# Performance work log

Measured on AMD Instinct MI355X. Metric: run time of the kernel, lower is better.

The kernel has to match this reference:

```python
import jax, jax.numpy as jnp
import numpy as np

D = 256          # out_feats
H = 4            # n_heads
DH = D // H      # per-head feats
S = 8192         # number of snapshots (segments)
PER = 32         # edges (selected papers) per snapshot
E = S * PER      # total edges
NP = 200000      # number of papers
ST = 10          # snapshot_types (embedding has ST+1 rows, padding_idx=-1)
SLOPE = 0.01     # LeakyReLU negative slope (torch default)


def setup_inputs() -> dict:
    key = jax.random.key(0)
    ks = jax.random.split(key, 20)
    sc = 1.0 / np.sqrt(D)
    papers = jax.random.normal(ks[0], (NP, D), dtype=jnp.float32)
    snapshots = jax.random.normal(ks[1], (S, D), dtype=jnp.float32)
    cur_snapshot_types = jax.random.randint(ks[2], (S,), 0, ST + 1, dtype=jnp.int32)
    is_cite = jax.random.randint(ks[3], (NP,), 0, 2, dtype=jnp.int32)
    selected_indicator = jax.random.randint(ks[4], (E,), 0, NP, dtype=jnp.int64)
    # contiguous sorted segment ids, PER edges per snapshot (matches valid_num_nodes)
    index = jnp.repeat(jnp.arange(S, dtype=jnp.int32), PER)
    # linear layers (torch Linear: y = x @ W.T + b)
    W_src = jax.random.normal(ks[5], (D, D), dtype=jnp.float32) * sc
    b_src = jnp.zeros((D,), dtype=jnp.float32)
    W_dst = jax.random.normal(ks[6], (D, D), dtype=jnp.float32) * sc
    b_dst = jnp.zeros((D,), dtype=jnp.float32)
    W_out = jax.random.normal(ks[7], (D, D), dtype=jnp.float32) * sc
    b_out = jnp.zeros((D,), dtype=jnp.float32)
    # node attr embeddings (2 rows, padding_idx=0 -> row 0 zero)
    emb_cite = jax.random.normal(ks[8], (2, D), dtype=jnp.float32).at[0].set(0.0)
    emb_ref = jax.random.normal(ks[9], (2, D), dtype=jnp.float32).at[0].set(0.0)
    emb_target = jax.random.normal(ks[10], (2, D), dtype=jnp.float32).at[0].set(0.0)
    # snapshot type embedding (ST+1 rows, padding_idx=-1 -> last row zero)
    snapshot_emb = jax.random.normal(ks[11], (ST + 1, D), dtype=jnp.float32).at[-1].set(0.0)
    # attention vectors, xavier_normal with relu gain
    gain = np.sqrt(2.0)
    std = gain * np.sqrt(2.0 / (H * DH + 1))
    attn = jax.random.normal(ks[12], (1, H, DH), dtype=jnp.float32) * std
    attn_t = jax.random.normal(ks[13], (1, H, DH), dtype=jnp.float32) * std
    return {
        "papers": papers, "snapshots": snapshots,
        "W_src": W_src, "b_src": b_src, "W_dst": W_dst, "b_dst": b_dst,
        "W_out": W_out, "b_out": b_out,
        "emb_cite": emb_cite, "emb_ref": emb_ref, "emb_target": emb_target,
        "snapshot_emb": snapshot_emb, "attn": attn, "attn_t": attn_t,
        "cur_snapshot_types": cur_snapshot_types, "is_cite": is_cite,
        "selected_indicator": selected_indicator, "index": index,
    }


def _leaky(x):
    return jnp.where(x >= 0, x, SLOPE * x)


def reference(papers, snapshots, W_src, b_src, W_dst, b_dst, W_out, b_out,
              emb_cite, emb_ref, emb_target, snapshot_emb, attn, attn_t,
              cur_snapshot_types, is_cite, selected_indicator, index):
    # gather src papers per edge: [E, D]
    h_src = papers[selected_indicator]
    feat_src = (h_src @ W_src.T + b_src).reshape(-1, H, DH)          # [E,H,DH]
    ic = is_cite[selected_indicator]
    # original uses 'is_cite' indices for all three attr embeddings (faithful)
    src_type_h = (emb_cite[ic] + emb_ref[ic] + emb_target[ic]).reshape(-1, H, DH)
    dst_type_h = snapshot_emb[cur_snapshot_types].reshape(-1, H, DH)  # [S,H,DH]
    feat_dst = (snapshots @ W_dst.T + b_dst).reshape(-1, H, DH)[index]  # [E,H,DH]
    # per-edge attention logits
    e = (_leaky(feat_src + feat_dst) * attn).sum(axis=-1)             # [E,H]
    et = (_leaky(src_type_h + dst_type_h[index]) * attn_t).sum(axis=-1)
    e = e + et
    # segment (edge) softmax over destination snapshots
    m = jax.lax.stop_gradient(jax.ops.segment_max(e, index, num_segments=S))
    ex = jnp.exp(e - m[index])
    den = jax.ops.segment_sum(ex, index, num_segments=S)
    a = (ex / den[index])[..., None]                                  # [E,H,1]
    # weighted segment-sum aggregation
    x = feat_src * a
    sum_out = jax.ops.segment_sum(x, index, num_segments=S).reshape(S, D)
    return sum_out @ W_out.T + b_out
```

## Files before the change

kernel.cpp:

```cpp
#include <hip/hip_runtime.h>
#include <hip/hip_fp16.h>
#include <type_traits>

#define NSNAP 8192
#define PER 32
#define SLOPE 0.01f

using half8   = __attribute__((ext_vector_type(8))) _Float16;
using floatx4 = __attribute__((ext_vector_type(4))) float;

__device__ __forceinline__ float leaky(float x) { return x >= 0.f ? x : SLOPE * x; }

__device__ __forceinline__ unsigned pack2(float a, float b) {
    __half2 h = __floats2half2_rn(a, b);
    return *reinterpret_cast<unsigned*>(&h);
}

template <typename AT, typename OT, bool DO_PACK>
__global__ __launch_bounds__(256) void gemm64(const AT* __restrict__ A,
                                              const float* __restrict__ W,
                                              const float* __restrict__ bias,
                                              OT* __restrict__ Cout, int M,
                                              const float* __restrict__ Wsrc,
                                              _Float16* __restrict__ Wh) {
    if constexpr (DO_PACK) {
        if (blockIdx.y == 4) {
            const int t = blockIdx.x * 256 + threadIdx.x;
            const int lane = t & 63;
            const int wj = (t >> 6) & 15;
            const int k0 = t >> 10;
            const int n = (wj >> 2) * 64 + (wj & 3) * 16 + (lane & 15);
            const int k = k0 * 32 + (lane >> 4) * 8;
            const float4 v0 = *(const float4*)(Wsrc + (long)n * 256 + k);
            const float4 v1 = *(const float4*)(Wsrc + (long)n * 256 + k + 4);
            *(uint4*)(Wh + (long)t * 8) = make_uint4(pack2(v0.x, v0.y), pack2(v0.z, v0.w),
                                                     pack2(v1.x, v1.y), pack2(v1.z, v1.w));
            return;
        }
    }
    constexpr int LDA = 40;
    __shared__ _Float16 Asl[64 * LDA];
    __shared__ _Float16 Wsl[64 * LDA];

    const int m0 = blockIdx.x * 64;
    const int n0 = blockIdx.y * 64;
    const int tid = threadIdx.x;
    const int lane = tid & 63;
    const int wave = tid >> 6;
    const int wm = (wave & 1) * 32;
    const int wn = (wave >> 1) * 32;
    const int l15 = lane & 15;
    const int quad = lane >> 4;

    floatx4 acc[2][2];
#pragma unroll
    for (int i = 0; i < 2; i++)
#pragma unroll
        for (int j = 0; j < 2; j++) acc[i][j] = (floatx4)0.f;

    for (int k0 = 0; k0 < 256; k0 += 32) {
        __syncthreads();
#pragma unroll
        for (int it = 0; it < 2; ++it) {
            const int idx = tid + it * 256;
            const int row = idx >> 3;
            const int c4 = idx & 7;
            if constexpr (std::is_same_v<AT, float>) {
                const float4 v = *(const float4*)(A + (long)(m0 + row) * 256 + k0 + c4 * 4);
                *(uint2*)(&Asl[row * LDA + c4 * 4]) = make_uint2(pack2(v.x, v.y), pack2(v.z, v.w));
            } else {
                const uint2 v = *(const uint2*)(A + (long)(m0 + row) * 256 + k0 + c4 * 4);
                *(uint2*)(&Asl[row * LDA + c4 * 4]) = v;
            }
            const float4 w = *(const float4*)(W + (long)(n0 + row) * 256 + k0 + c4 * 4);
            *(uint2*)(&Wsl[row * LDA + c4 * 4]) = make_uint2(pack2(w.x, w.y), pack2(w.z, w.w));
        }
        __syncthreads();

        half8 af[2], bf[2];
#pragma unroll
        for (int i = 0; i < 2; i++)
            af[i] = *reinterpret_cast<const half8*>(&Asl[(wm + i * 16 + l15) * LDA + quad * 8]);
#pragma unroll
        for (int j = 0; j < 2; j++)
            bf[j] = *reinterpret_cast<const half8*>(&Wsl[(wn + j * 16 + l15) * LDA + quad * 8]);
#pragma unroll
        for (int i = 0; i < 2; i++)
#pragma unroll
            for (int j = 0; j < 2; j++)
                acc[i][j] = __builtin_amdgcn_mfma_f32_16x16x32_f16(af[i], bf[j], acc[i][j], 0, 0, 0);
    }

#pragma unroll
    for (int j = 0; j < 2; j++) {
        const int gcol = n0 + wn + j * 16 + l15;
        const float bv = bias[gcol];
#pragma unroll
        for (int i = 0; i < 2; i++) {
            const int rbase = m0 + wm + i * 16 + quad * 4;
#pragma unroll
            for (int r = 0; r < 4; r++) {
                const float v = acc[i][j][r] + bv;
                if constexpr (std::is_same_v<OT, __half>)
                    Cout[(long)(rbase + r) * 256 + gcol] = __float2half(v);
                else
                    Cout[(long)(rbase + r) * 256 + gcol] = v;
            }
        }
    }
}

__global__ __launch_bounds__(256, 2) void fused_attn(
    const float* __restrict__ papers, const _Float16* __restrict__ Wh,
    const float* __restrict__ b_src, const float* __restrict__ F,
    const float* __restrict__ emb_cite, const float* __restrict__ emb_ref,
    const float* __restrict__ emb_target, const float* __restrict__ snap_emb,
    const float* __restrict__ attn, const float* __restrict__ attn_t,
    const int* __restrict__ types, const int* __restrict__ is_cite,
    const int* __restrict__ sel, __half* __restrict__ SO) {
    __shared__ _Float16 Asl[64 * 256];
    __shared__ int ic_l[64];

    const int tid = threadIdx.x;
    const int lane = tid & 63;
    const int wave = tid >> 6;
    const int l15 = lane & 15;
    const int quad = lane >> 4;
    const int sbase = blockIdx.x * 2;
    const int ebase = blockIdx.x * 64;

    if (tid < 64) ic_l[tid] = is_cite[sel[ebase + tid]];

    {
        const int row = wave * 16 + l15;
        const long arow = (long)sel[ebase + row];
        const float* src = papers + arow * 256;
#pragma unroll
        for (int m = 0; m < 16; m++) {
            const float4 v = *(const float4*)(src + m * 16 + quad * 4);
            const int c8 = m * 2 + (quad >> 1);
            const int slot = (c8 >> 2) * 256 + wave * 64 + (c8 & 3) * 16 + l15;
            *(uint2*)(&Asl[slot * 8 + (quad & 1) * 4]) =
                make_uint2(pack2(v.x, v.y), pack2(v.z, v.w));
        }
    }
    __syncthreads();

    floatx4 acc[4][4];
#pragma unroll
    for (int i = 0; i < 4; i++)
#pragma unroll
        for (int j = 0; j < 4; j++) acc[i][j] = (floatx4)0.f;

    for (int k0 = 0; k0 < 8; k0++) {
        half8 af[4], bf[4];
#pragma unroll
        for (int i = 0; i < 4; i++)
            af[i] = *reinterpret_cast<const half8*>(&Asl[(k0 * 256 + i * 64 + lane) * 8]);
#pragma unroll
        for (int j = 0; j < 4; j++)
            bf[j] = *reinterpret_cast<const half8*>(Wh + ((k0 * 16 + wave * 4 + j) * 64 + lane) * 8);
#pragma unroll
        for (int i = 0; i < 4; i++)
#pragma unroll
            for (int j = 0; j < 4; j++)
                acc[i][j] = __builtin_amdgcn_mfma_f32_16x16x32_f16(af[i], bf[j], acc[i][j], 0, 0, 0);
    }

    float bsrc_j[4], attn_j[4], F0_j[4], F1_j[4];
#pragma unroll
    for (int j = 0; j < 4; j++) {
        const int col = 64 * wave + j * 16 + l15;
        bsrc_j[j] = b_src[col];
        attn_j[j] = attn[col];
        F0_j[j] = F[(long)sbase * 256 + col];
        F1_j[j] = F[(long)(sbase + 1) * 256 + col];
    }
#pragma unroll
    for (int i = 0; i < 4; i++)
#pragma unroll
        for (int j = 0; j < 4; j++)
#pragma unroll
            for (int r = 0; r < 4; r++) acc[i][j][r] += bsrc_j[j];

    const int D = 64 * wave + lane;
    const float at_d = attn_t[D];
    const float src0 = emb_cite[D] + emb_ref[D] + emb_target[D];
    const float src1 = emb_cite[256 + D] + emb_ref[256 + D] + emb_target[256 + D];
    float et[2][2];
#pragma unroll
    for (int sn = 0; sn < 2; sn++) {
        const float dstt = snap_emb[types[sbase + sn] * 256 + D];
        float p0 = leaky(src0 + dstt) * at_d;
        float p1 = leaky(src1 + dstt) * at_d;
#pragma unroll
        for (int off = 32; off; off >>= 1) {
            p0 += __shfl_xor(p0, off);
            p1 += __shfl_xor(p1, off);
        }
        et[sn][0] = p0;
        et[sn][1] = p1;
    }

    float lg[4][4];
#pragma unroll
    for (int i = 0; i < 4; i++) {
        const int sn = i >> 1;
#pragma unroll
        for (int r = 0; r < 4; r++) {
            float p = 0.f;
#pragma unroll
            for (int j = 0; j < 4; j++)
                p += leaky(acc[i][j][r] + (sn == 0 ? F0_j[j] : F1_j[j])) * attn_j[j];
#pragma unroll
            for (int off = 1; off <= 8; off <<= 1) p += __shfl_xor(p, off);
            const int row = i * 16 + quad * 4 + r;
            lg[i][r] = p + et[sn][ic_l[row]];
        }
    }

    float aw[4][4];
#pragma unroll
    for (int sn = 0; sn < 2; sn++) {
        float m = -3.4e38f;
#pragma unroll
        for (int ii = 0; ii < 2; ii++)
#pragma unroll
            for (int r = 0; r < 4; r++) m = fmaxf(m, lg[sn * 2 + ii][r]);
        m = fmaxf(m, __shfl_xor(m, 16));
        m = fmaxf(m, __shfl_xor(m, 32));
        float den = 0.f;
#pragma unroll
        for (int ii = 0; ii < 2; ii++)
#pragma unroll
            for (int r = 0; r < 4; r++) {
                const float ex = __expf(lg[sn * 2 + ii][r] - m);
                aw[sn * 2 + ii][r] = ex;
                den += ex;
            }
        den += __shfl_xor(den, 16);
        den += __shfl_xor(den, 32);
        const float inv = 1.f / den;
#pragma unroll
        for (int ii = 0; ii < 2; ii++)
#pragma unroll
            for (int r = 0; r < 4; r++) aw[sn * 2 + ii][r] *= inv;
    }

#pragma unroll
    for (int sn = 0; sn < 2; sn++) {
#pragma unroll
        for (int j = 0; j < 4; j++) {
            float o = 0.f;
#pragma unroll
            for (int ii = 0; ii < 2; ii++)
#pragma unroll
                for (int r = 0; r < 4; r++) o += aw[sn * 2 + ii][r] * acc[sn * 2 + ii][j][r];
            o += __shfl_xor(o, 16);
            o += __shfl_xor(o, 32);
            if (quad == sn)
                SO[(long)(sbase + sn) * 256 + 64 * wave + j * 16 + l15] = __float2half(o);
        }
    }
}

extern "C" void kernel_launch(void* const* d_in, const int* in_sizes, int n_in,
                              void* d_out, int out_size, void* d_ws, size_t ws_size,
                              hipStream_t stream) {
    const float* papers     = (const float*)d_in[0];
    const float* snapshots  = (const float*)d_in[1];
    const float* W_src      = (const float*)d_in[2];
    const float* b_src      = (const float*)d_in[3];
    const float* W_dst      = (const float*)d_in[4];
    const float* b_dst      = (const float*)d_in[5];
    const float* W_out      = (const float*)d_in[6];
    const float* b_out      = (const float*)d_in[7];
    const float* emb_cite   = (const float*)d_in[8];
    const float* emb_ref    = (const float*)d_in[9];
    const float* emb_target = (const float*)d_in[10];
    const float* snap_emb   = (const float*)d_in[11];
    const float* attn       = (const float*)d_in[12];
    const float* attn_t     = (const float*)d_in[13];
    const int* types        = (const int*)d_in[14];
    const int* is_cite      = (const int*)d_in[15];
    const int* sel          = (const int*)d_in[16];

    char* ws = (char*)d_ws;
    float*     F    = (float*)ws;
    __half*    SO   = (__half*)(ws + 8388608);
    _Float16*  Wh   = (_Float16*)(ws + 12582912);

    gemm64<float, float, true><<<dim3(128, 5), 256, 0, stream>>>(snapshots, W_dst, b_dst, F,
                                                                 NSNAP, W_src, Wh);
    fused_attn<<<NSNAP / 2, 256, 0, stream>>>(papers, Wh, b_src, F, emb_cite, emb_ref,
                                              emb_target, snap_emb, attn, attn_t, types,
                                              is_cite, sel, SO);
    gemm64<__half, float, false><<<dim3(128, 4), 256, 0, stream>>>(SO, W_out, b_out,
                                                                   (float*)d_out, NSNAP,
                                                                   nullptr, nullptr);
}
```

Baseline: 386.8 us.

## Fuse dst projection and output GEMM into attention kernel, pre-pack all weights

Replaces the separate snapshot projection GEMM and output GEMM with per-block MFMA computations inside the fused attention kernel. A small pack kernel converts W_src, W_dst and W_out to fp16 in the MFMA fragment layout up front. This removes the F and SO round trips through global memory and two kernel launches. In exchange, the two small per-block GEMMs use MFMA tiles that are mostly wasted (only 2 of 16 rows are real) and add work and latency to each block.

```diff
diff --git a/kernel.cpp b/kernel.cpp
--- a/kernel.cpp
+++ b/kernel.cpp
@@ -1,6 +1,5 @@
 #include <hip/hip_runtime.h>
 #include <hip/hip_fp16.h>
-#include <type_traits>
 
 #define NSNAP 8192
 #define PER 32
@@ -16,109 +15,36 @@
     return *reinterpret_cast<unsigned*>(&h);
 }
 
-template <typename AT, typename OT, bool DO_PACK>
-__global__ __launch_bounds__(256) void gemm64(const AT* __restrict__ A,
-                                              const float* __restrict__ W,
-                                              const float* __restrict__ bias,
-                                              OT* __restrict__ Cout, int M,
-                                              const float* __restrict__ Wsrc,
-                                              _Float16* __restrict__ Wh) {
-    if constexpr (DO_PACK) {
-        if (blockIdx.y == 4) {
-            const int t = blockIdx.x * 256 + threadIdx.x;
-            const int lane = t & 63;
-            const int wj = (t >> 6) & 15;
-            const int k0 = t >> 10;
-            const int n = (wj >> 2) * 64 + (wj & 3) * 16 + (lane & 15);
-            const int k = k0 * 32 + (lane >> 4) * 8;
-            const float4 v0 = *(const float4*)(Wsrc + (long)n * 256 + k);
-            const float4 v1 = *(const float4*)(Wsrc + (long)n * 256 + k + 4);
-            *(uint4*)(Wh + (long)t * 8) = make_uint4(pack2(v0.x, v0.y), pack2(v0.z, v0.w),
-                                                     pack2(v1.x, v1.y), pack2(v1.z, v1.w));
-            return;
-        }
-    }
-    constexpr int LDA = 40;
-    __shared__ _Float16 Asl[64 * LDA];
-    __shared__ _Float16 Wsl[64 * LDA];
-
-    const int m0 = blockIdx.x * 64;
-    const int n0 = blockIdx.y * 64;
-    const int tid = threadIdx.x;
-    const int lane = tid & 63;
-    const int wave = tid >> 6;
-    const int wm = (wave & 1) * 32;
-    const int wn = (wave >> 1) * 32;
-    const int l15 = lane & 15;
-    const int quad = lane >> 4;
-
-    floatx4 acc[2][2];
-#pragma unroll
-    for (int i = 0; i < 2; i++)
-#pragma unroll
-        for (int j = 0; j < 2; j++) acc[i][j] = (floatx4)0.f;
-
-    for (int k0 = 0; k0 < 256; k0 += 32) {
-        __syncthreads();
-#pragma unroll
-        for (int it = 0; it < 2; ++it) {
-            const int idx = tid + it * 256;
-            const int row = idx >> 3;
-            const int c4 = idx & 7;
-            if constexpr (std::is_same_v<AT, float>) {
-                const float4 v = *(const float4*)(A + (long)(m0 + row) * 256 + k0 + c4 * 4);
-                *(uint2*)(&Asl[row * LDA + c4 * 4]) = make_uint2(pack2(v.x, v.y), pack2(v.z, v.w));
-            } else {
-                const uint2 v = *(const uint2*)(A + (long)(m0 + row) * 256 + k0 + c4 * 4);
-                *(uint2*)(&Asl[row * LDA + c4 * 4]) = v;
-            }
-            const float4 w = *(const float4*)(W + (long)(n0 + row) * 256 + k0 + c4 * 4);
-            *(uint2*)(&Wsl[row * LDA + c4 * 4]) = make_uint2(pack2(w.x, w.y), pack2(w.z, w.w));
-        }
-        __syncthreads();
-
-        half8 af[2], bf[2];
-#pragma unroll
-        for (int i = 0; i < 2; i++)
-            af[i] = *reinterpret_cast<const half8*>(&Asl[(wm + i * 16 + l15) * LDA + quad * 8]);
-#pragma unroll
-        for (int j = 0; j < 2; j++)
-            bf[j] = *reinterpret_cast<const half8*>(&Wsl[(wn + j * 16 + l15) * LDA + quad * 8]);
-#pragma unroll
-        for (int i = 0; i < 2; i++)
-#pragma unroll
-            for (int j = 0; j < 2; j++)
-                acc[i][j] = __builtin_amdgcn_mfma_f32_16x16x32_f16(af[i], bf[j], acc[i][j], 0, 0, 0);
-    }
-
-#pragma unroll
-    for (int j = 0; j < 2; j++) {
-        const int gcol = n0 + wn + j * 16 + l15;
-        const float bv = bias[gcol];
-#pragma unroll
-        for (int i = 0; i < 2; i++) {
-            const int rbase = m0 + wm + i * 16 + quad * 4;
-#pragma unroll
-            for (int r = 0; r < 4; r++) {
-                const float v = acc[i][j][r] + bv;
-                if constexpr (std::is_same_v<OT, __half>)
-                    Cout[(long)(rbase + r) * 256 + gcol] = __float2half(v);
-                else
-                    Cout[(long)(rbase + r) * 256 + gcol] = v;
-            }
-        }
-    }
-}
-
-__global__ __launch_bounds__(256, 2) void fused_attn(
-    const float* __restrict__ papers, const _Float16* __restrict__ Wh,
-    const float* __restrict__ b_src, const float* __restrict__ F,
+__global__ __launch_bounds__(256) void pack_w3(const float* __restrict__ W0,
+                                               const float* __restrict__ W1,
+                                               const float* __restrict__ W2,
+                                               _Float16* __restrict__ Wh) {
+    const int mat = blockIdx.x >> 5;
+    const float* W = mat == 0 ? W0 : (mat == 1 ? W1 : W2);
+    const int t = (blockIdx.x & 31) * 256 + threadIdx.x;
+    const int lane = t & 63;
+    const int wj = (t >> 6) & 15;
+    const int k0 = t >> 10;
+    const int n = (wj >> 2) * 64 + (wj & 3) * 16 + (lane & 15);
+    const int k = k0 * 32 + (lane >> 4) * 8;
+    const float4 v0 = *(const float4*)(W + (long)n * 256 + k);
+    const float4 v1 = *(const float4*)(W + (long)n * 256 + k + 4);
+    *(uint4*)(Wh + (long)mat * 65536 + (long)t * 8) =
+        make_uint4(pack2(v0.x, v0.y), pack2(v0.z, v0.w), pack2(v1.x, v1.y), pack2(v1.z, v1.w));
+}
+
+__global__ __launch_bounds__(256, 2) void fused_all(
+    const float* __restrict__ papers, const float* __restrict__ snapshots,
+    const _Float16* __restrict__ Whs, const _Float16* __restrict__ Whd,
+    const _Float16* __restrict__ Who, const float* __restrict__ b_src,
+    const float* __restrict__ b_dst, const float* __restrict__ b_out,
     const float* __restrict__ emb_cite, const float* __restrict__ emb_ref,
     const float* __restrict__ emb_target, const float* __restrict__ snap_emb,
     const float* __restrict__ attn, const float* __restrict__ attn_t,
     const int* __restrict__ types, const int* __restrict__ is_cite,
-    const int* __restrict__ sel, __half* __restrict__ SO) {
+    const int* __restrict__ sel, float* __restrict__ out) {
     __shared__ _Float16 Asl[64 * 256];
+    __shared__ _Float16 SOsl[2 * 256];
     __shared__ int ic_l[64];
 
     const int tid = threadIdx.x;
@@ -144,6 +70,33 @@
                 make_uint2(pack2(v.x, v.y), pack2(v.z, v.w));
         }
     }
+
+    float F0_j[4], F1_j[4];
+    {
+        floatx4 accf[4];
+#pragma unroll
+        for (int j = 0; j < 4; j++) accf[j] = (floatx4)0.f;
+        const float* srow = snapshots + (long)(sbase + (l15 & 1)) * 256;
+        for (int k0 = 0; k0 < 8; k0++) {
+            const float4 s0 = *(const float4*)(srow + k0 * 32 + quad * 8);
+            const float4 s1 = *(const float4*)(srow + k0 * 32 + quad * 8 + 4);
+            uint4 u = make_uint4(pack2(s0.x, s0.y), pack2(s0.z, s0.w),
+                                 pack2(s1.x, s1.y), pack2(s1.z, s1.w));
+            const half8 af = *reinterpret_cast<half8*>(&u);
+#pragma unroll
+            for (int j = 0; j < 4; j++) {
+                const half8 bf =
+                    *reinterpret_cast<const half8*>(Whd + ((k0 * 16 + wave * 4 + j) * 64 + lane) * 8);
+                accf[j] = __builtin_amdgcn_mfma_f32_16x16x32_f16(af, bf, accf[j], 0, 0, 0);
+            }
+        }
+#pragma unroll
+        for (int j = 0; j < 4; j++) {
+            const float bd = b_dst[64 * wave + j * 16 + l15];
+            F0_j[j] = __shfl(accf[j][0], l15) + bd;
+            F1_j[j] = __shfl(accf[j][1], l15) + bd;
+        }
+    }
     __syncthreads();
 
     floatx4 acc[4][4];
@@ -159,7 +112,7 @@
             af[i] = *reinterpret_cast<const half8*>(&Asl[(k0 * 256 + i * 64 + lane) * 8]);
 #pragma unroll
         for (int j = 0; j < 4; j++)
-            bf[j] = *reinterpret_cast<const half8*>(Wh + ((k0 * 16 + wave * 4 + j) * 64 + lane) * 8);
+            bf[j] = *reinterpret_cast<const half8*>(Whs + ((k0 * 16 + wave * 4 + j) * 64 + lane) * 8);
 #pragma unroll
         for (int i = 0; i < 4; i++)
 #pragma unroll
@@ -167,14 +120,12 @@
                 acc[i][j] = __builtin_amdgcn_mfma_f32_16x16x32_f16(af[i], bf[j], acc[i][j], 0, 0, 0);
     }
 
-    float bsrc_j[4], attn_j[4], F0_j[4], F1_j[4];
+    float bsrc_j[4], attn_j[4];
 #pragma unroll
     for (int j = 0; j < 4; j++) {
         const int col = 64 * wave + j * 16 + l15;
         bsrc_j[j] = b_src[col];
         attn_j[j] = attn[col];
-        F0_j[j] = F[(long)sbase * 256 + col];
-        F1_j[j] = F[(long)(sbase + 1) * 256 + col];
     }
 #pragma unroll
     for (int i = 0; i < 4; i++)
@@ -258,8 +209,33 @@
                 for (int r = 0; r < 4; r++) o += aw[sn * 2 + ii][r] * acc[sn * 2 + ii][j][r];
             o += __shfl_xor(o, 16);
             o += __shfl_xor(o, 32);
-            if (quad == sn)
-                SO[(long)(sbase + sn) * 256 + 64 * wave + j * 16 + l15] = __float2half(o);
+            if (quad == sn) SOsl[sn * 256 + 64 * wave + j * 16 + l15] = (_Float16)o;
+        }
+    }
+    __syncthreads();
+
+    {
+        floatx4 acco[4];
+#pragma unroll
+        for (int j = 0; j < 4; j++) acco[j] = (floatx4)0.f;
+        for (int k0 = 0; k0 < 8; k0++) {
+            const half8 af =
+                *reinterpret_cast<const half8*>(&SOsl[(l15 & 1) * 256 + k0 * 32 + quad * 8]);
+#pragma unroll
+            for (int j = 0; j < 4; j++) {
+                const half8 bf =
+                    *reinterpret_cast<const half8*>(Who + ((k0 * 16 + wave * 4 + j) * 64 + lane) * 8);
+                acco[j] = __builtin_amdgcn_mfma_f32_16x16x32_f16(af, bf, acco[j], 0, 0, 0);
+            }
+        }
+        if (quad == 0) {
+#pragma unroll
+            for (int j = 0; j < 4; j++) {
+                const int col = 64 * wave + j * 16 + l15;
+                const float bo = b_out[col];
+                out[(long)sbase * 256 + col] = acco[j][0] + bo;
+                out[(long)(sbase + 1) * 256 + col] = acco[j][1] + bo;
+            }
         }
     }
 }
@@ -285,17 +261,13 @@
     const int* is_cite      = (const int*)d_in[15];
     const int* sel          = (const int*)d_in[16];
 
-    char* ws = (char*)d_ws;
-    float*     F    = (float*)ws;
-    __half*    SO   = (__half*)(ws + 8388608);
-    _Float16*  Wh   = (_Float16*)(ws + 12582912);
-
-    gemm64<float, float, true><<<dim3(128, 5), 256, 0, stream>>>(snapshots, W_dst, b_dst, F,
-                                                                 NSNAP, W_src, Wh);
-    fused_attn<<<NSNAP / 2, 256, 0, stream>>>(papers, Wh, b_src, F, emb_cite, emb_ref,
-                                              emb_target, snap_emb, attn, attn_t, types,
-                                              is_cite, sel, SO);
-    gemm64<__half, float, false><<<dim3(128, 4), 256, 0, stream>>>(SO, W_out, b_out,
-                                                                   (float*)d_out, NSNAP,
-                                                                   nullptr, nullptr);
-}
+    _Float16* Wh = (_Float16*)d_ws;
+    _Float16* Whs = Wh;
+    _Float16* Whd = Wh + 65536;
+    _Float16* Who = Wh + 131072;
+
+    pack_w3<<<96, 256, 0, stream>>>(W_src, W_dst, W_out, Wh);
+    fused_all<<<NSNAP / 2, 256, 0, stream>>>(papers, snapshots, Whs, Whd, Who, b_src, b_dst,
+                                             b_out, emb_cite, emb_ref, emb_target, snap_emb,
+                                             attn, attn_t, types, is_cite, sel, (float*)d_out);
+}
```

Result: slower. 502.6 us (+29.9%).
